# Kernel tuning notes

Hardware: AMD Instinct MI355X
Metric: run time of the kernel (lower is better)

The kernel has to match this reference:

```python
import jax, jax.numpy as jnp
import numpy as np
from jax import lax

LOW_T = 0.01
HIGH_T = 0.05
KSIZE = 1
SIGMA = 1.5
D, H, W = 128, 512, 512


def _gauss_kernel(k, sigma):
    c = k // 2
    ii, jj = np.meshgrid(np.arange(k), np.arange(k), indexing='ij')
    ker = np.exp(-((ii - c) ** 2 + (jj - c) ** 2) / (2.0 * sigma ** 2)).astype(np.float32)
    return ker / ker.sum()


def setup_inputs() -> dict:
    key = jax.random.key(0)
    x = jax.random.normal(key, (D, H, W), dtype=jnp.float32)
    gk = jnp.asarray(_gauss_kernel(KSIZE, SIGMA))[None, None]  # [1,1,k,k]
    sobel_x = jnp.asarray([[[[-1, 0, 1], [-2, 0, 2], [-1, 0, 1]]]], dtype=jnp.float32)
    sobel_y = jnp.asarray([[[[-1, -2, -1], [0, 0, 0], [1, 2, 1]]]], dtype=jnp.float32)
    return {"x": x, "gk": gk, "sobel_x": sobel_x, "sobel_y": sobel_y}


def _conv(x, k):
    # cross-correlation, padding=1, matches F.conv2d(..., padding=1)
    return lax.conv_general_dilated(x, k, (1, 1), [(1, 1), (1, 1)],
                                    dimension_numbers=('NCHW', 'OIHW', 'NCHW'))


def reference(x, gk, sobel_x, sobel_y):
    d, h, w = x.shape
    xb = x[:, None]                       # [D,1,H,W] -> batch over slices
    xs = _conv(xb, gk)                    # 1x1 gaussian + pad=1 grows to H+2,W+2
    gx = _conv(xs, sobel_x)
    gy = _conv(xs, sobel_y)
    mag = jnp.sqrt(gx * gx + gy * gy)[:, 0]   # [D,H',W']
    ang = jnp.arctan2(gy, gx)[:, 0]

    # quantized angle: round-half-to-even matches torch.round
    q = jnp.mod(jnp.round(ang / (np.pi / 4.0)) * 45.0, 180.0)
    r = lambda s: jnp.roll(mag, s, axis=(1, 2))
    keep_h = (mag >= r((0, 1))) & (mag >= r((0, -1)))
    keep_v = (mag >= r((1, 0))) & (mag >= r((-1, 0)))
    keep_45 = (mag >= r((1, 1))) & (mag >= r((-1, -1)))
    keep_135 = (mag >= r((1, -1))) & (mag >= r((-1, 1)))
    keep = jnp.where(q == 90.0, keep_v,
           jnp.where(q == 45.0, keep_45,
           jnp.where(q == 135.0, keep_135, keep_h)))
    mag = jnp.where(keep, mag, jnp.float32(0.0))

    # double threshold, per-slice global max (original computes max per 2D slice)
    high = jnp.max(mag, axis=(1, 2), keepdims=True) * HIGH_T
    low = high * LOW_T
    strong = jnp.where(mag >= high, 1.0, 0.0).astype(jnp.float32)
    weak = jnp.where((mag <= high) & (mag >= low), 0.5, 0.0).astype(jnp.float32)

    # hysteresis: 3x3 max-pool stride 1 pad 1
    pooled = lax.reduce_window(strong, -jnp.inf, lax.max, (1, 3, 3), (1, 1, 1),
                               [(0, 0), (1, 1), (1, 1)])
    edges = jnp.where((pooled == 1.0) & (weak == 0.5), 1.0, strong)

    # trim back to input spatial size (centered), mirroring forward()
    dh = edges.shape[1] - h
    dw = edges.shape[2] - w
    if dh > 0:
        edges = edges[:, dh // 2: edges.shape[1] - (dh - dh // 2), :]
    if dw > 0:
        edges = edges[:, :, dw // 2: edges.shape[2] - (dw - dw // 2)]
    return edges
```

## Files before the change

### kernel.cpp

```cpp
#include <hip/hip_runtime.h>
#include <math.h>

#define DD 128
#define HW 512
#define MG 514


static __device__ float fd_atanf(float x) {
    #pragma clang fp contract(off)
    const unsigned hx = __float_as_uint(x);
    const unsigned ix = hx & 0x7fffffffu;
    const double A0 = 0.46364760900080611621425623146121440203;
    const double A1 = 0.78539816339744830961566084581987572105;
    const double A2 = 0.98279372324732906798571061101466601449;
    const double A3 = 1.57079632679489661923132169163975144210;
    const float aT0 =  3.3333328366e-01f;
    const float aT1 = -1.9999158382e-01f;
    const float aT2 =  1.4253635705e-01f;
    const float aT3 = -1.0648017377e-01f;
    const float aT4 =  6.1687607318e-02f;
    float z, w, s1, s2;
    int id;
    double a;
    if (ix >= 0x4c800000u) {
        a = A3;
        float hi = (float)a; if ((double)hi > a) hi = __uint_as_float(__float_as_uint(hi) - 1u);
        float lo = (float)(a - (double)hi);
        float r = hi + lo;
        return (hx >> 31) ? -r : r;
    }
    if (ix < 0x3ee00000u) {
        if (ix < 0x39800000u) return x;
        id = -1;
    } else {
        x = fabsf(x);
        if (ix < 0x3f980000u) {
            if (ix < 0x3f300000u) { id = 0; x = (2.0f * x - 1.0f) / (2.0f + x); }
            else                  { id = 1; x = (x - 1.0f) / (x + 1.0f); }
        } else {
            if (ix < 0x401c0000u) { id = 2; x = (x - 1.5f) / (1.0f + 1.5f * x); }
            else                  { id = 3; x = -1.0f / x; }
        }
    }
    z = x * x;
    w = z * z;
    s1 = z * (aT0 + w * (aT2 + w * aT4));
    s2 = w * (aT1 + w * aT3);
    if (id < 0) return x - x * (s1 + s2);
    a = (id == 0) ? A0 : (id == 1) ? A1 : (id == 2) ? A2 : A3;
    float hi = (float)a; if ((double)hi > a) hi = __uint_as_float(__float_as_uint(hi) - 1u);
    float lo = (float)(a - (double)hi);
    z = hi - ((x * (s1 + s2) - lo) - x);
    return (hx >> 31) ? -z : z;
}

static __device__ __noinline__ int cls_fd(float y, float x) {
    #pragma clang fp contract(off)
    const unsigned hx = __float_as_uint(x), hy = __float_as_uint(y);
    const unsigned ix = hx & 0x7fffffffu, iy = hy & 0x7fffffffu;
    unsigned m = ((hy >> 31) & 1u) | ((hx >> 30) & 2u);
    const double PI_D = 3.14159265358979323846264338327950288420;
    const float pi_f  = (float)PI_D;
    const float pi_lo = (float)(PI_D - (double)pi_f);
    const float pi4_f = (float)(PI_D / 4.0);
    const float pi2_f = (float)(PI_D / 2.0);
    float v;
    if (iy == 0) {
        v = (m == 0 || m == 1) ? y : (m == 2 ? pi_f : -pi_f);
    } else if (ix == 0) {
        v = (m & 1u) ? -pi2_f : pi2_f;
    } else if (ix + (26u << 23) < iy) {
        v = (m & 1u) ? -pi2_f : pi2_f;
    } else {
        float z;
        if ((m & 2u) && iy + (26u << 23) < ix) z = 0.0f;
        else z = fd_atanf(fabsf(y / x));
        switch (m) {
            case 0:  v = z; break;
            case 1:  v = -z; break;
            case 2:  v = pi_f - (z - pi_lo); break;
            default: v = (z - pi_lo) - pi_f; break;
        }
    }
    float t = v / pi4_f;
    int n = (int)rintf(t);
    return n & 3;
}

static __device__ __forceinline__ int classify(float gx, float gy) {
    #pragma clang fp contract(off)
    float ax = fabsf(gx), ay = fabsf(gy);
    const float T = 0.41421356237309504880f;
    float r1 = ay - ax * T;
    float r2 = ax - ay * T;
    float eps = 1e-4f * (ax + ay);
    if (fabsf(r1) > eps && fabsf(r2) > eps) {
        if (r1 < 0.0f) return 0;
        if (r2 < 0.0f) return 2;
        return ((__float_as_uint(gx) ^ __float_as_uint(gy)) >> 31) ? 3 : 1;
    }
    return cls_fd(gy, gx);
}

static __device__ __forceinline__ void grad_g1v(float x00, float x01, float x02,
                                                float x10, float x12,
                                                float x20, float x21, float x22,
                                                float& gx, float& gy) {
    #pragma clang fp contract(off)
    { float A = -x00; float B = x02 + (-x20); float C = 2.0f*x12; float D = -2.0f*x10;
      float E = A + B; float F = C + D; gx = (E + F) + x22; }
    { float A = -x00; float B = (-x02) + x20; float C = -2.0f*x01; float D = 2.0f*x21;
      float E = A + B; float F = C + D; gy = (E + F) + x22; }
}

static __device__ __forceinline__ float mag2(float gx, float gy) {
    #pragma clang fp contract(off)
    float p = gx * gx;
    float q = gy * gy;
    return sqrtf(p + q);
}
static __device__ __forceinline__ float sq2(float gx, float gy) {
    #pragma clang fp contract(off)
    float p = gx * gx;
    float q = gy * gy;
    return p + q;
}

#define LOADROW(S_, ROWEXPR) do {                                                     \
    int Rx_ = (ROWEXPR);                                                              \
    int W_ = Rx_;  W_ += (W_ < 0) ? MG : 0;  W_ -= (W_ >= MG) ? MG : 0;               \
    float4 xv_ = float4{0.f, 0.f, 0.f, 0.f}; float hv_ = 0.f;                         \
    if ((unsigned)(W_ - 1) < (unsigned)HW) {                                          \
        const float* rowp_ = xd + (size_t)(W_ - 1) * HW;                              \
        xv_ = *(const float4*)(rowp_ + j0 + 4 * lane);                                \
        if (hland && hok) hv_ = rowp_[hcolv];                                         \
    }                                                                                 \
    float hA_ = __shfl(hv_, 0),  hB_ = __shfl(hv_, 1),  hC_ = __shfl(hv_, 2);         \
    float hD_ = __shfl(hv_, 61), hE_ = __shfl(hv_, 62), hF_ = __shfl(hv_, 63);        \
    float xlv_ = __shfl_up(xv_.w, 1);   if (L0)  xlv_ = hC_;                          \
    float xrv_ = __shfl_down(xv_.x, 1); if (L63) xrv_ = hD_;                          \
    Xc0[S_] = xv_.x; Xc1[S_] = xv_.y; Xc2[S_] = xv_.z; Xc3[S_] = xv_.w;               \
    Xl[S_] = xlv_; Xr[S_] = xrv_;                                                     \
    E0[S_] = L0 ? hA_ : hD_; E1[S_] = L0 ? hB_ : hE_; E2[S_] = L0 ? hC_ : hF_;        \
} while (0)

#define MAGS6_F(u0, u1, u2, MAGFN)                                                    \
    float gx0, gy0, gx1, gy1, gx2, gy2, gx3, gy3;                                     \
    grad_g1v(Xl[u0], Xc0[u0], Xc1[u0], Xl[u1], Xc1[u1],                               \
             Xl[u2], Xc0[u2], Xc1[u2], gx0, gy0);                                     \
    grad_g1v(Xc0[u0], Xc1[u0], Xc2[u0], Xc0[u1], Xc2[u1],                             \
             Xc0[u2], Xc1[u2], Xc2[u2], gx1, gy1);                                    \
    grad_g1v(Xc1[u0], Xc2[u0], Xc3[u0], Xc1[u1], Xc3[u1],                             \
             Xc1[u2], Xc2[u2], Xc3[u2], gx2, gy2);                                    \
    grad_g1v(Xc2[u0], Xc3[u0], Xr[u0], Xc2[u1], Xr[u1],                               \
             Xc2[u2], Xc3[u2], Xr[u2], gx3, gy3);                                     \
    float m0_ = MAGFN(gx0, gy0), m1_ = MAGFN(gx1, gy1);                               \
    float m2_ = MAGFN(gx2, gy2), m3_ = MAGFN(gx3, gy3);                               \
    float A0_ = L0 ? E0[u0] : Xc3[u0], B0_ = L0 ? E1[u0] : E0[u0];                    \
    float C0_ = L0 ? E2[u0] : E1[u0],  D0_ = L0 ? Xc0[u0] : E2[u0];                   \
    float A1_ = L0 ? E0[u1] : Xc3[u1], B1_ = L0 ? E1[u1] : E0[u1];                    \
    float C1_ = L0 ? E2[u1] : E1[u1],  D1_ = L0 ? Xc0[u1] : E2[u1];                   \
    float A2_ = L0 ? E0[u2] : Xc3[u2], B2_ = L0 ? E1[u2] : E0[u2];                    \
    float C2_ = L0 ? E2[u2] : E1[u2],  D2_ = L0 ? Xc0[u2] : E2[u2];                   \
    float g1x, g1y, g2x, g2y;                                                         \
    grad_g1v(A0_, B0_, C0_, A1_, C1_, A2_, B2_, C2_, g1x, g1y);                       \
    grad_g1v(B0_, C0_, D0_, B1_, D1_, B2_, C2_, D2_, g2x, g2y);                       \
    float em1 = MAGFN(g1x, g1y), em2 = MAGFN(g2x, g2y);

#define M1BODY(kk, S, DOMAG) do {                                                     \
    constexpr int s_ = (S);                                                           \
    constexpr int u0 = (s_ + 1) % 3, u1 = (s_ + 2) % 3, u2 = s_;                      \
    LOADROW(s_, h0m - 1 + (kk));                                                      \
    if (DOMAG) {                                                                      \
        int Rm = h0m - 2 + (kk);                                                      \
        if (Rm <= 513) {                                                              \
            MAGS6_F(u0, u1, u2, sq2)                                                  \
            acc = fmaxf(acc, fmaxf(fmaxf(m0_, m1_), fmaxf(m2_, m3_)));                \
            if (L0 || L63) acc = fmaxf(acc, fmaxf(em1, em2));                         \
        }                                                                             \
    }                                                                                 \
} while (0)

__global__ __launch_bounds__(256) void k_max1(const float* __restrict__ x,
                                              unsigned int* __restrict__ smax) {
    const int lane = threadIdx.x, ty = threadIdx.y;
    const int d  = blockIdx.z;
    const int j0 = blockIdx.x * 256;
    const int h0m = (blockIdx.y * 4 + ty) * 33;
    const float* xd = x + (size_t)d * HW * HW;
    const bool L0 = (lane == 0), L63 = (lane == 63);
    const bool hland = (lane < 3) | (lane >= 61);
    int hg = j0 + ((lane < 3) ? (lane - 2) : (lane + 196));
    hg += (hg < 0) ? MG : 0;  hg -= (hg >= MG) ? MG : 0;
    const bool hok   = (unsigned)(hg - 1) < (unsigned)HW;
    const int  hcolv = hok ? (hg - 1) : 0;

    float Xc0[3], Xc1[3], Xc2[3], Xc3[3], Xl[3], Xr[3], E0[3], E1[3], E2[3];
    float acc = 0.0f;

    M1BODY(0, 0, 0); M1BODY(1, 1, 0);
    #pragma unroll
    for (int kb = 2; kb < 35; kb += 3) {
        M1BODY(kb + 0, 2, 1);
        M1BODY(kb + 1, 0, 1);
        M1BODY(kb + 2, 1, 1);
    }

    for (int off = 32; off > 0; off >>= 1)
        acc = fmaxf(acc, __shfl_down(acc, off, 64));
    if (lane == 0) {
        float mx = sqrtf(acc);
        atomicMax(smax + d, __float_as_uint(mx));
    }
}

#define P2BODY(kk, S, DO_MAG, DO_NMS, DO_OUT) do {                                    \
    constexpr int s_ = (S);                                                           \
    constexpr int sp1 = (s_ + 1) % 3, sp2 = (s_ + 2) % 3;                             \
    LOADROW(s_, h0 - 3 + (kk));                                                       \
    if (DO_MAG) {                                                                     \
        MAGS6_F(sp1, sp2, s_, mag2)                                                   \
        float mlv = __shfl_up(m3_, 1);   if (L0)  mlv = em2;                          \
        float mrv = __shfl_down(m0_, 1); if (L63) mrv = em1;                          \
        M0[sp1] = m0_; M1[sp1] = m1_; M2[sp1] = m2_; M3[sp1] = m3_;                   \
        Mlft[sp1] = mlv; Mrgt[sp1] = mrv;                                             \
        Emc[sp1] = L0 ? em2 : em1;                                                    \
        Eml[sp1] = L0 ? em1 : m3_;                                                    \
        Emr[sp1] = L0 ? m0_ : em2;                                                    \
        C0[sp1] = classify(gx0, gy0); C1[sp1] = classify(gx1, gy1);                   \
        C2[sp1] = classify(gx2, gy2); C3[sp1] = classify(gx3, gy3);                   \
        Ecl[sp1] = classify(L0 ? g2x : g1x, L0 ? g2y : g1y);                          \
    }                                                                                 \
    if (DO_NMS) {                                                                     \
        constexpr int w0 = sp2, w1 = s_, w2 = sp1;                                    \
        float n0_, n1_, n2_, n3_;                                                     \
        { float m = M0[w1]; int c = C0[w1];                                           \
          float a = (c==0)?Mlft[w1]:(c==1)?Mlft[w0]:(c==2)?M0[w0]:M1[w0];             \
          float b = (c==0)?M1[w1]:(c==1)?M1[w2]:(c==2)?M0[w2]:Mlft[w2];               \
          n0_ = (m >= a && m >= b) ? m : 0.0f; }                                      \
        { float m = M1[w1]; int c = C1[w1];                                           \
          float a = (c==0)?M0[w1]:(c==1)?M0[w0]:(c==2)?M1[w0]:M2[w0];                 \
          float b = (c==0)?M2[w1]:(c==1)?M2[w2]:(c==2)?M1[w2]:M0[w2];                 \
          n1_ = (m >= a && m >= b) ? m : 0.0f; }                                      \
        { float m = M2[w1]; int c = C2[w1];                                           \
          float a = (c==0)?M1[w1]:(c==1)?M1[w0]:(c==2)?M2[w0]:M3[w0];                 \
          float b = (c==0)?M3[w1]:(c==1)?M3[w2]:(c==2)?M2[w2]:M1[w2];                 \
          n2_ = (m >= a && m >= b) ? m : 0.0f; }                                      \
        { float m = M3[w1]; int c = C3[w1];                                           \
          float a = (c==0)?M2[w1]:(c==1)?M2[w0]:(c==2)?M3[w0]:Mrgt[w0];               \
          float b = (c==0)?Mrgt[w1]:(c==1)?Mrgt[w2]:(c==2)?M3[w2]:M2[w2];             \
          n3_ = (m >= a && m >= b) ? m : 0.0f; }                                      \
        float env;                                                                    \
        { float m = Emc[w1]; int c = Ecl[w1];                                         \
          float a = (c==0)?Eml[w1]:(c==1)?Eml[w0]:(c==2)?Emc[w0]:Emr[w0];             \
          float b = (c==0)?Emr[w1]:(c==1)?Emr[w2]:(c==2)?Emc[w2]:Eml[w2];             \
          env = (m >= a && m >= b) ? m : 0.0f; }                                      \
        float nlv = __shfl_up(n3_, 1);   if (L0)  nlv = env;                          \
        float nrv = __shfl_down(n0_, 1); if (L63) nrv = env;                          \
        N0[sp2] = n0_; N1[sp2] = n1_; N2[sp2] = n2_; N3[sp2] = n3_;                   \
        Nl[sp2] = nlv; Nr[sp2] = nrv;                                                 \
    }                                                                                 \
    if (DO_OUT) {                                                                     \
        constexpr int z0 = s_, z1 = sp1, z2 = sp2;                                    \
        int Rh = h0 + (kk) - 6;                                                       \
        float4 e4;                                                                    \
        { float m = N0[z1]; float e;                                                  \
          if (m >= high) e = 1.0f;                                                    \
          else if (m >= low) {                                                        \
            bool p = Nl[z0]>=high || N0[z0]>=high || N1[z0]>=high ||                  \
                     Nl[z1]>=high ||                  N1[z1]>=high ||                 \
                     Nl[z2]>=high || N0[z2]>=high || N1[z2]>=high;                    \
            e = p ? 1.0f : 0.0f; } else e = 0.0f;                                     \
          e4.x = e; }                                                                 \
        { float m = N1[z1]; float e;                                                  \
          if (m >= high) e = 1.0f;                                                    \
          else if (m >= low) {                                                        \
            bool p = N0[z0]>=high || N1[z0]>=high || N2[z0]>=high ||                  \
                     N0[z1]>=high ||                  N2[z1]>=high ||                 \
                     N0[z2]>=high || N1[z2]>=high || N2[z2]>=high;                    \
            e = p ? 1.0f : 0.0f; } else e = 0.0f;                                     \
          e4.y = e; }                                                                 \
        { float m = N2[z1]; float e;                                                  \
          if (m >= high) e = 1.0f;                                                    \
          else if (m >= low) {                                                        \
            bool p = N1[z0]>=high || N2[z0]>=high || N3[z0]>=high ||                  \
                     N1[z1]>=high ||                  N3[z1]>=high ||                 \
                     N1[z2]>=high || N2[z2]>=high || N3[z2]>=high;                    \
            e = p ? 1.0f : 0.0f; } else e = 0.0f;                                     \
          e4.z = e; }                                                                 \
        { float m = N3[z1]; float e;                                                  \
          if (m >= high) e = 1.0f;                                                    \
          else if (m >= low) {                                                        \
            bool p = N2[z0]>=high || N3[z0]>=high || Nr[z0]>=high ||                  \
                     N2[z1]>=high ||                  Nr[z1]>=high ||                 \
                     N2[z2]>=high || N3[z2]>=high || Nr[z2]>=high;                    \
            e = p ? 1.0f : 0.0f; } else e = 0.0f;                                     \
          e4.w = e; }                                                                 \
        if (Rh <= 512)                                                                \
            *(float4*)(od + (size_t)(Rh - 1) * HW + j0 + 4 * lane) = e4;              \
    }                                                                                 \
} while (0)

__global__ __launch_bounds__(256) void k_fused(const float* __restrict__ x,
                                               const unsigned int* __restrict__ smax,
                                               float* __restrict__ out) {
    const int lane = threadIdx.x, ty = threadIdx.y;
    const int d  = blockIdx.z;
    const int j0 = blockIdx.x * 256;
    const int h0 = 1 + (blockIdx.y * 4 + ty) * 22;
    const float* xd = x + (size_t)d * HW * HW;
    float* od = out + (size_t)d * HW * HW;
    const bool L0 = (lane == 0), L63 = (lane == 63);
    const bool hland = (lane < 3) | (lane >= 61);
    int hg = j0 + ((lane < 3) ? (lane - 2) : (lane + 196));
    hg += (hg < 0) ? MG : 0;  hg -= (hg >= MG) ? MG : 0;
    const bool hok   = (unsigned)(hg - 1) < (unsigned)HW;
    const int  hcolv = hok ? (hg - 1) : 0;

    const float high = __uint_as_float(smax[d]) * 0.05f;
    const float low  = high * 0.01f;

    float Xc0[3], Xc1[3], Xc2[3], Xc3[3], Xl[3], Xr[3], E0[3], E1[3], E2[3];
    float M0[3], M1[3], M2[3], M3[3], Mlft[3], Mrgt[3], Emc[3], Eml[3], Emr[3];
    int   C0[3], C1[3], C2[3], C3[3], Ecl[3];
    float N0[3], N1[3], N2[3], N3[3], Nl[3], Nr[3];

    P2BODY(0, 0, 0, 0, 0);
    P2BODY(1, 1, 0, 0, 0);
    P2BODY(2, 2, 1, 0, 0);
    P2BODY(3, 0, 1, 0, 0);
    P2BODY(4, 1, 1, 1, 0);
    P2BODY(5, 2, 1, 1, 0);
    #pragma unroll 1
    for (int kb = 6; kb < 27; kb += 3) {
        P2BODY(kb + 0, 0, 1, 1, 1);
        P2BODY(kb + 1, 1, 1, 1, 1);
        P2BODY(kb + 2, 2, 1, 1, 1);
    }
    P2BODY(27, 0, 1, 1, 1);
}

extern "C" void kernel_launch(void* const* d_in, const int* in_sizes, int n_in,
                              void* d_out, int out_size, void* d_ws, size_t ws_size,
                              hipStream_t stream) {
    const float* x = (const float*)d_in[0];
    float* out = (float*)d_out;
    unsigned int* smax = (unsigned int*)d_ws;

    hipMemsetAsync(smax, 0, DD * sizeof(unsigned int), stream);

    dim3 blk(64, 4, 1);
    k_max1 <<<dim3(2, 4, DD), blk, 0, stream>>>(x, smax);
    k_fused<<<dim3(2, 6, DD), blk, 0, stream>>>(x, smax, out);
}
```

Before: 168.0 us.

## Widen max-pass rows per lane, bit-pack NMS classes and strong masks

The max pass now has each lane load two float4s (8 columns) so one wavefront covers a full 512-wide row. Each warp handles 9 rows, and the launch uses 15 row-blocks per slice, replacing the halo-shuffle scheme and giving more blocks in flight. In the fused kernel, the four direction classes plus the edge class are packed into one register, and strong-pixel flags become a bitmask per row. Hysteresis is then done with a bitwise OR and shift dilation instead of many float compares. This cuts register pressure and ALU work, but the max pass now reads halo rows more often.

```diff
diff --git a/kernel.cpp b/kernel.cpp
--- a/kernel.cpp
+++ b/kernel.cpp
@@ -126,6 +126,84 @@
     return p + q;
 }
 
+#define M1LOAD(S_, ROWEXPR) do {                                                      \
+    int W_ = (ROWEXPR); W_ += (W_ < 0) ? MG : 0; W_ -= (W_ >= MG) ? MG : 0;           \
+    float4 a_ = {0.f,0.f,0.f,0.f}, b_ = {0.f,0.f,0.f,0.f};                            \
+    if ((unsigned)(W_ - 1) < (unsigned)HW) {                                          \
+        const float* rp_ = xd + (size_t)(W_ - 1) * HW + 8 * lane;                     \
+        a_ = *(const float4*)rp_;  b_ = *(const float4*)(rp_ + 4);                    \
+    }                                                                                 \
+    X0[S_]=a_.x; X1[S_]=a_.y; X2[S_]=a_.z; X3[S_]=a_.w;                               \
+    X4[S_]=b_.x; X5[S_]=b_.y; X6[S_]=b_.z; X7[S_]=b_.w;                               \
+    float xl_ = __shfl_up(b_.w, 1);   if (L0)  xl_ = 0.0f;                            \
+    float xr_ = __shfl_down(a_.x, 1); if (L63) xr_ = 0.0f;                            \
+    Xl[S_] = xl_; Xr[S_] = xr_;                                                       \
+    B0[S_] = __shfl(a_.x, 0);  B7[S_] = __shfl(b_.w, 63);                             \
+} while (0)
+
+#define M1G(p0,p1,p2,q1,r0,r1,r2) do {                                                \
+    float gx_, gy_;                                                                   \
+    grad_g1v(p0, p1, p2, q1##a, q1##b, r0, r1, r2, gx_, gy_);                         \
+    acc = fmaxf(acc, sq2(gx_, gy_));                                                  \
+} while (0)
+
+#define M1BODY(kk, S, DOMAG) do {                                                     \
+    constexpr int s_ = (S);                                                           \
+    constexpr int u0 = (s_ + 1) % 3, u1 = (s_ + 2) % 3, u2 = s_;                      \
+    M1LOAD(s_, h0m - 1 + (kk));                                                       \
+    if (DOMAG) {                                                                      \
+        int Rm = h0m - 2 + (kk);                                                      \
+        if (Rm <= 513) {                                                              \
+            float gx_, gy_;                                                           \
+            grad_g1v(Xl[u0],X0[u0],X1[u0], Xl[u1],X1[u1], Xl[u2],X0[u2],X1[u2],gx_,gy_); \
+            acc = fmaxf(acc, sq2(gx_, gy_));                                          \
+            grad_g1v(X0[u0],X1[u0],X2[u0], X0[u1],X2[u1], X0[u2],X1[u2],X2[u2],gx_,gy_); \
+            acc = fmaxf(acc, sq2(gx_, gy_));                                          \
+            grad_g1v(X1[u0],X2[u0],X3[u0], X1[u1],X3[u1], X1[u2],X2[u2],X3[u2],gx_,gy_); \
+            acc = fmaxf(acc, sq2(gx_, gy_));                                          \
+            grad_g1v(X2[u0],X3[u0],X4[u0], X2[u1],X4[u1], X2[u2],X3[u2],X4[u2],gx_,gy_); \
+            acc = fmaxf(acc, sq2(gx_, gy_));                                          \
+            grad_g1v(X3[u0],X4[u0],X5[u0], X3[u1],X5[u1], X3[u2],X4[u2],X5[u2],gx_,gy_); \
+            acc = fmaxf(acc, sq2(gx_, gy_));                                          \
+            grad_g1v(X4[u0],X5[u0],X6[u0], X4[u1],X6[u1], X4[u2],X5[u2],X6[u2],gx_,gy_); \
+            acc = fmaxf(acc, sq2(gx_, gy_));                                          \
+            grad_g1v(X5[u0],X6[u0],X7[u0], X5[u1],X7[u1], X5[u2],X6[u2],X7[u2],gx_,gy_); \
+            acc = fmaxf(acc, sq2(gx_, gy_));                                          \
+            grad_g1v(X6[u0],X7[u0],Xr[u0], X6[u1],Xr[u1], X6[u2],X7[u2],Xr[u2],gx_,gy_); \
+            acc = fmaxf(acc, sq2(gx_, gy_));                                          \
+                     \
+            grad_g1v(0.0f,0.0f,B0[u0], 0.0f,B0[u1], 0.0f,0.0f,B0[u2], gx_, gy_);      \
+            acc = fmaxf(acc, sq2(gx_, gy_));                                          \
+            grad_g1v(B7[u0],0.0f,0.0f, B7[u1],0.0f, B7[u2],0.0f,0.0f, gx_, gy_);      \
+            acc = fmaxf(acc, sq2(gx_, gy_));                                          \
+        }                                                                             \
+    }                                                                                 \
+} while (0)
+
+__global__ __launch_bounds__(256) void k_max1(const float* __restrict__ x,
+                                              unsigned int* __restrict__ smax) {
+    const int lane = threadIdx.x, ty = threadIdx.y;
+    const int d  = blockIdx.z;
+    const int h0m = (blockIdx.y * 4 + ty) * 9;
+    const float* xd = x + (size_t)d * HW * HW;
+    const bool L0 = (lane == 0), L63 = (lane == 63);
+
+    float X0[3],X1[3],X2[3],X3[3],X4[3],X5[3],X6[3],X7[3],Xl[3],Xr[3],B0[3],B7[3];
+    float acc = 0.0f;
+
+    M1BODY(0, 0, 0);  M1BODY(1, 1, 0);
+    M1BODY(2, 2, 1);  M1BODY(3, 0, 1);  M1BODY(4, 1, 1);
+    M1BODY(5, 2, 1);  M1BODY(6, 0, 1);  M1BODY(7, 1, 1);
+    M1BODY(8, 2, 1);  M1BODY(9, 0, 1);  M1BODY(10, 1, 1);
+
+    for (int off = 32; off > 0; off >>= 1)
+        acc = fmaxf(acc, __shfl_down(acc, off, 64));
+    if (lane == 0) {
+        float mx = sqrtf(acc);
+        atomicMax(smax + d, __float_as_uint(mx));
+    }
+}
+
 #define LOADROW(S_, ROWEXPR) do {                                                     \
     int Rx_ = (ROWEXPR);                                                              \
     int W_ = Rx_;  W_ += (W_ < 0) ? MG : 0;  W_ -= (W_ >= MG) ? MG : 0;               \
@@ -167,53 +245,6 @@
     grad_g1v(B0_, C0_, D0_, B1_, D1_, B2_, C2_, D2_, g2x, g2y);                       \
     float em1 = MAGFN(g1x, g1y), em2 = MAGFN(g2x, g2y);
 
-#define M1BODY(kk, S, DOMAG) do {                                                     \
-    constexpr int s_ = (S);                                                           \
-    constexpr int u0 = (s_ + 1) % 3, u1 = (s_ + 2) % 3, u2 = s_;                      \
-    LOADROW(s_, h0m - 1 + (kk));                                                      \
-    if (DOMAG) {                                                                      \
-        int Rm = h0m - 2 + (kk);                                                      \
-        if (Rm <= 513) {                                                              \
-            MAGS6_F(u0, u1, u2, sq2)                                                  \
-            acc = fmaxf(acc, fmaxf(fmaxf(m0_, m1_), fmaxf(m2_, m3_)));                \
-            if (L0 || L63) acc = fmaxf(acc, fmaxf(em1, em2));                         \
-        }                                                                             \
-    }                                                                                 \
-} while (0)
-
-__global__ __launch_bounds__(256) void k_max1(const float* __restrict__ x,
-                                              unsigned int* __restrict__ smax) {
-    const int lane = threadIdx.x, ty = threadIdx.y;
-    const int d  = blockIdx.z;
-    const int j0 = blockIdx.x * 256;
-    const int h0m = (blockIdx.y * 4 + ty) * 33;
-    const float* xd = x + (size_t)d * HW * HW;
-    const bool L0 = (lane == 0), L63 = (lane == 63);
-    const bool hland = (lane < 3) | (lane >= 61);
-    int hg = j0 + ((lane < 3) ? (lane - 2) : (lane + 196));
-    hg += (hg < 0) ? MG : 0;  hg -= (hg >= MG) ? MG : 0;
-    const bool hok   = (unsigned)(hg - 1) < (unsigned)HW;
-    const int  hcolv = hok ? (hg - 1) : 0;
-
-    float Xc0[3], Xc1[3], Xc2[3], Xc3[3], Xl[3], Xr[3], E0[3], E1[3], E2[3];
-    float acc = 0.0f;
-
-    M1BODY(0, 0, 0); M1BODY(1, 1, 0);
-    #pragma unroll
-    for (int kb = 2; kb < 35; kb += 3) {
-        M1BODY(kb + 0, 2, 1);
-        M1BODY(kb + 1, 0, 1);
-        M1BODY(kb + 2, 1, 1);
-    }
-
-    for (int off = 32; off > 0; off >>= 1)
-        acc = fmaxf(acc, __shfl_down(acc, off, 64));
-    if (lane == 0) {
-        float mx = sqrtf(acc);
-        atomicMax(smax + d, __float_as_uint(mx));
-    }
-}
-
 #define P2BODY(kk, S, DO_MAG, DO_NMS, DO_OUT) do {                                    \
     constexpr int s_ = (S);                                                           \
     constexpr int sp1 = (s_ + 1) % 3, sp2 = (s_ + 2) % 3;                             \
@@ -227,75 +258,63 @@
         Emc[sp1] = L0 ? em2 : em1;                                                    \
         Eml[sp1] = L0 ? em1 : m3_;                                                    \
         Emr[sp1] = L0 ? m0_ : em2;                                                    \
-        C0[sp1] = classify(gx0, gy0); C1[sp1] = classify(gx1, gy1);                   \
-        C2[sp1] = classify(gx2, gy2); C3[sp1] = classify(gx3, gy3);                   \
-        Ecl[sp1] = classify(L0 ? g2x : g1x, L0 ? g2y : g1y);                          \
+        unsigned cp_ = (unsigned)classify(gx0, gy0)                                   \
+                     | ((unsigned)classify(gx1, gy1) << 2)                            \
+                     | ((unsigned)classify(gx2, gy2) << 4)                            \
+                     | ((unsigned)classify(gx3, gy3) << 6)                            \
+                     | ((unsigned)classify(L0 ? g2x : g1x, L0 ? g2y : g1y) << 8);     \
+        CP[sp1] = cp_;                                                                \
     }                                                                                 \
     if (DO_NMS) {                                                                     \
         constexpr int w0 = sp2, w1 = s_, w2 = sp1;                                    \
+        unsigned cpv = CP[w1];                                                        \
         float n0_, n1_, n2_, n3_;                                                     \
-        { float m = M0[w1]; int c = C0[w1];                                           \
+        { float m = M0[w1]; int c = cpv & 3;                                          \
           float a = (c==0)?Mlft[w1]:(c==1)?Mlft[w0]:(c==2)?M0[w0]:M1[w0];             \
           float b = (c==0)?M1[w1]:(c==1)?M1[w2]:(c==2)?M0[w2]:Mlft[w2];               \
           n0_ = (m >= a && m >= b) ? m : 0.0f; }                                      \
-        { float m = M1[w1]; int c = C1[w1];                                           \
+        { float m = M1[w1]; int c = (cpv >> 2) & 3;                                   \
           float a = (c==0)?M0[w1]:(c==1)?M0[w0]:(c==2)?M1[w0]:M2[w0];                 \
           float b = (c==0)?M2[w1]:(c==1)?M2[w2]:(c==2)?M1[w2]:M0[w2];                 \
           n1_ = (m >= a && m >= b) ? m : 0.0f; }                                      \
-        { float m = M2[w1]; int c = C2[w1];                                           \
+        { float m = M2[w1]; int c = (cpv >> 4) & 3;                                   \
           float a = (c==0)?M1[w1]:(c==1)?M1[w0]:(c==2)?M2[w0]:M3[w0];                 \
           float b = (c==0)?M3[w1]:(c==1)?M3[w2]:(c==2)?M2[w2]:M1[w2];                 \
           n2_ = (m >= a && m >= b) ? m : 0.0f; }                                      \
-        { float m = M3[w1]; int c = C3[w1];                                           \
+        { float m = M3[w1]; int c = (cpv >> 6) & 3;                                   \
           float a = (c==0)?M2[w1]:(c==1)?M2[w0]:(c==2)?M3[w0]:Mrgt[w0];               \
           float b = (c==0)?Mrgt[w1]:(c==1)?Mrgt[w2]:(c==2)?M3[w2]:M2[w2];             \
           n3_ = (m >= a && m >= b) ? m : 0.0f; }                                      \
         float env;                                                                    \
-        { float m = Emc[w1]; int c = Ecl[w1];                                         \
+        { float m = Emc[w1]; int c = (cpv >> 8) & 3;                                  \
           float a = (c==0)?Eml[w1]:(c==1)?Eml[w0]:(c==2)?Emc[w0]:Emr[w0];             \
           float b = (c==0)?Emr[w1]:(c==1)?Emr[w2]:(c==2)?Emc[w2]:Eml[w2];             \
           env = (m >= a && m >= b) ? m : 0.0f; }                                      \
-        float nlv = __shfl_up(n3_, 1);   if (L0)  nlv = env;                          \
-        float nrv = __shfl_down(n0_, 1); if (L63) nrv = env;                          \
+        unsigned sm_ = (n0_ >= high ? 1u : 0u) | (n1_ >= high ? 2u : 0u)              \
+                     | (n2_ >= high ? 4u : 0u) | (n3_ >= high ? 8u : 0u);             \
+        unsigned eb_ = (env >= high) ? 1u : 0u;                                       \
+        unsigned su_ = (unsigned)__shfl_up((int)sm_, 1);                              \
+        unsigned sd_ = (unsigned)__shfl_down((int)sm_, 1);                            \
+        unsigned lb_ = L0 ? eb_ : ((su_ >> 3) & 1u);                                  \
+        unsigned rb_ = L63 ? eb_ : (sd_ & 1u);                                        \
         N0[sp2] = n0_; N1[sp2] = n1_; N2[sp2] = n2_; N3[sp2] = n3_;                   \
-        Nl[sp2] = nlv; Nr[sp2] = nrv;                                                 \
+        Rm[sp2] = lb_ | (sm_ << 1) | (rb_ << 5);                                      \
     }                                                                                 \
     if (DO_OUT) {                                                                     \
         constexpr int z0 = s_, z1 = sp1, z2 = sp2;                                    \
         int Rh = h0 + (kk) - 6;                                                       \
+        unsigned comb = Rm[z0] | Rm[z1] | Rm[z2];                                     \
+        unsigned dil  = comb | (comb << 1) | (comb >> 1);                             \
+        unsigned srow = Rm[z1];                                                       \
         float4 e4;                                                                    \
-        { float m = N0[z1]; float e;                                                  \
-          if (m >= high) e = 1.0f;                                                    \
-          else if (m >= low) {                                                        \
-            bool p = Nl[z0]>=high || N0[z0]>=high || N1[z0]>=high ||                  \
-                     Nl[z1]>=high ||                  N1[z1]>=high ||                 \
-                     Nl[z2]>=high || N0[z2]>=high || N1[z2]>=high;                    \
-            e = p ? 1.0f : 0.0f; } else e = 0.0f;                                     \
-          e4.x = e; }                                                                 \
-        { float m = N1[z1]; float e;                                                  \
-          if (m >= high) e = 1.0f;                                                    \
-          else if (m >= low) {                                                        \
-            bool p = N0[z0]>=high || N1[z0]>=high || N2[z0]>=high ||                  \
-                     N0[z1]>=high ||                  N2[z1]>=high ||                 \
-                     N0[z2]>=high || N1[z2]>=high || N2[z2]>=high;                    \
-            e = p ? 1.0f : 0.0f; } else e = 0.0f;                                     \
-          e4.y = e; }                                                                 \
-        { float m = N2[z1]; float e;                                                  \
-          if (m >= high) e = 1.0f;                                                    \
-          else if (m >= low) {                                                        \
-            bool p = N1[z0]>=high || N2[z0]>=high || N3[z0]>=high ||                  \
-                     N1[z1]>=high ||                  N3[z1]>=high ||                 \
-                     N1[z2]>=high || N2[z2]>=high || N3[z2]>=high;                    \
-            e = p ? 1.0f : 0.0f; } else e = 0.0f;                                     \
-          e4.z = e; }                                                                 \
-        { float m = N3[z1]; float e;                                                  \
-          if (m >= high) e = 1.0f;                                                    \
-          else if (m >= low) {                                                        \
-            bool p = N2[z0]>=high || N3[z0]>=high || Nr[z0]>=high ||                  \
-                     N2[z1]>=high ||                  Nr[z1]>=high ||                 \
-                     N2[z2]>=high || N3[z2]>=high || Nr[z2]>=high;                    \
-            e = p ? 1.0f : 0.0f; } else e = 0.0f;                                     \
-          e4.w = e; }                                                                 \
+        e4.x = (((srow >> 1) & 1u) | (((dil >> 1) & 1u) & (N0[z1] >= low ? 1u : 0u))) \
+               ? 1.0f : 0.0f;                                                         \
+        e4.y = (((srow >> 2) & 1u) | (((dil >> 2) & 1u) & (N1[z1] >= low ? 1u : 0u))) \
+               ? 1.0f : 0.0f;                                                         \
+        e4.z = (((srow >> 3) & 1u) | (((dil >> 3) & 1u) & (N2[z1] >= low ? 1u : 0u))) \
+               ? 1.0f : 0.0f;                                                         \
+        e4.w = (((srow >> 4) & 1u) | (((dil >> 4) & 1u) & (N3[z1] >= low ? 1u : 0u))) \
+               ? 1.0f : 0.0f;                                                         \
         if (Rh <= 512)                                                                \
             *(float4*)(od + (size_t)(Rh - 1) * HW + j0 + 4 * lane) = e4;              \
     }                                                                                 \
@@ -322,8 +341,8 @@
 
     float Xc0[3], Xc1[3], Xc2[3], Xc3[3], Xl[3], Xr[3], E0[3], E1[3], E2[3];
     float M0[3], M1[3], M2[3], M3[3], Mlft[3], Mrgt[3], Emc[3], Eml[3], Emr[3];
-    int   C0[3], C1[3], C2[3], C3[3], Ecl[3];
-    float N0[3], N1[3], N2[3], N3[3], Nl[3], Nr[3];
+    unsigned CP[3], Rm[3];
+    float N0[3], N1[3], N2[3], N3[3];
 
     P2BODY(0, 0, 0, 0, 0);
     P2BODY(1, 1, 0, 0, 0);
@@ -350,6 +369,6 @@
     hipMemsetAsync(smax, 0, DD * sizeof(unsigned int), stream);
 
     dim3 blk(64, 4, 1);
-    k_max1 <<<dim3(2, 4, DD), blk, 0, stream>>>(x, smax);
+    k_max1 <<<dim3(1, 15, DD), blk, 0, stream>>>(x, smax);
     k_fused<<<dim3(2, 6, DD), blk, 0, stream>>>(x, smax, out);
 }
```

Measured after the change: 172.0 us. 1.02x slower.
